# Kernel tuning notes

Measured on AMD Instinct MI355X. Metric: run time of the kernel, lower is better.

## Reference

```python
import jax, jax.numpy as jnp
import numpy as np

B, N, IN, OUT, H, F = 4, 2048, 128, 64, 4, 64


def setup_inputs() -> dict:
    key = jax.random.key(0)
    ks = jax.random.split(key, 10)
    h = jax.random.normal(ks[0], (B, N, IN), dtype=jnp.float32)
    projection_matrix = jax.random.uniform(ks[1], (B, N, N), dtype=jnp.float32)
    similarity_matrix = jnp.tanh(jax.random.normal(ks[2], (B, N, N), dtype=jnp.float32))
    quadrant_matrix = jax.random.randint(ks[3], (B, N, N, 2), 0, 4)
    # learned params (xavier-ish scaling); stored as (in, out) so x @ W
    W = jax.random.normal(ks[4], (IN, OUT * H), dtype=jnp.float32) * (1.0 / np.sqrt(IN))
    random_projection = jax.random.normal(ks[5], (IN, F), dtype=jnp.float32) * 0.1
    a_q = jax.random.normal(ks[6], (2 * F, OUT), dtype=jnp.float32) * (1.0 / np.sqrt(2 * F))
    a_k = jax.random.normal(ks[7], (2 * F, OUT), dtype=jnp.float32) * (1.0 / np.sqrt(2 * F))
    quadrant_bias = jax.random.normal(ks[8], (4, 4), dtype=jnp.float32) * 0.02
    output_proj = jax.random.normal(ks[9], (OUT * H, OUT), dtype=jnp.float32) * (1.0 / np.sqrt(OUT * H))
    return {
        "h": h,
        "projection_matrix": projection_matrix,
        "similarity_matrix": similarity_matrix,
        "W": W,
        "random_projection": random_projection,
        "a_q": a_q,
        "a_k": a_k,
        "quadrant_bias": quadrant_bias,
        "output_proj": output_proj,
        "quadrant_matrix": quadrant_matrix,
    }


def reference(h, projection_matrix, similarity_matrix, W, random_projection,
              a_q, a_k, quadrant_bias, output_proj, quadrant_matrix):
    # random feature map: phi = [cos(h R), sin(h R)]  -> (B, N, 2F)
    proj = jnp.einsum('bnd,df->bnf', h, random_projection)
    phi = jnp.concatenate([jnp.cos(proj), jnp.sin(proj)], axis=-1)
    Q = phi @ a_q                       # (B, N, OUT)
    K = phi @ a_k                       # (B, N, OUT)
    Wh = (h @ W).reshape(h.shape[0], h.shape[1], H, OUT)  # (B, N, H, OUT)

    scores = jnp.einsum('bio,bjo->bij', Q, K)             # (B, N, N)
    # additive relational biases (shared across heads)
    qb = quadrant_bias[quadrant_matrix[..., 0], quadrant_matrix[..., 1]]  # (B, N, N)
    scores = scores + projection_matrix + similarity_matrix + qb
    attn = jax.nn.softmax(scores[:, None, :, :], axis=-1)  # (B, H, N, N) via broadcast

    # aggregate values per head, then concat heads
    hp = jnp.einsum('bhij,bjhk->bihk', attn, Wh)           # (B, N, H, OUT)
    hp = hp.reshape(h.shape[0], h.shape[1], H * OUT)
    out = hp @ output_proj                                  # (B, N, OUT)
    return jax.nn.elu(out)
```

## Files before the change

kernel.cpp:

```cpp
#include <hip/hip_runtime.h>
#include <math.h>

#define BB   4
#define NN   2048
#define IND  128
#define CDIM 256
#define NIT  16

typedef _Float16 half_t;
typedef _Float16 half4_t __attribute__((ext_vector_type(4)));
typedef _Float16 half8_t __attribute__((ext_vector_type(8)));
typedef float    f32x4   __attribute__((ext_vector_type(4)));

#define SHIFT 16.0f

__global__ __launch_bounds__(256) void precompute_kernel(
    const float* __restrict__ hg,
    const float* __restrict__ W,
    const float* __restrict__ R,
    const float* __restrict__ aq,
    const float* __restrict__ ak,
    half_t* __restrict__ Qw,
    half_t* __restrict__ Kw,
    half_t* __restrict__ WhJ)
{
    const int tid  = threadIdx.x;
    const int row0 = blockIdx.x * 8;

    __shared__ float hs[8][IND];
    __shared__ float phis[8][IND];

    {
        const float4* src = (const float4*)(hg + (size_t)row0 * IND);
        ((float4*)&hs[0][0])[tid] = src[tid];
    }
    __syncthreads();

    {
        const int f  = tid & 63;
        const int rr = tid >> 6;
        float p0 = 0.f, p1 = 0.f;
        #pragma unroll 4
        for (int d0 = 0; d0 < IND; d0 += 4) {
            const float r0 = R[(d0 + 0) * 64 + f];
            const float r1 = R[(d0 + 1) * 64 + f];
            const float r2 = R[(d0 + 2) * 64 + f];
            const float r3 = R[(d0 + 3) * 64 + f];
            const float4 ha = *(const float4*)&hs[rr][d0];
            const float4 hb = *(const float4*)&hs[rr + 4][d0];
            p0 += ha.x * r0 + ha.y * r1 + ha.z * r2 + ha.w * r3;
            p1 += hb.x * r0 + hb.y * r1 + hb.z * r2 + hb.w * r3;
        }
        float s, c;
        __sincosf(p0, &s, &c); phis[rr][f]     = c; phis[rr][f + 64]     = s;
        __sincosf(p1, &s, &c); phis[rr + 4][f] = c; phis[rr + 4][f + 64] = s;
    }

    {
        float acc[8];
        #pragma unroll
        for (int r = 0; r < 8; ++r) acc[r] = 0.f;
        #pragma unroll 2
        for (int d0 = 0; d0 < IND; d0 += 4) {
            const float w0 = W[(d0 + 0) * CDIM + tid];
            const float w1 = W[(d0 + 1) * CDIM + tid];
            const float w2 = W[(d0 + 2) * CDIM + tid];
            const float w3 = W[(d0 + 3) * CDIM + tid];
            #pragma unroll
            for (int r = 0; r < 8; ++r) {
                const float4 h4 = *(const float4*)&hs[r][d0];
                acc[r] += h4.x * w0 + h4.y * w1 + h4.z * w2 + h4.w * w3;
            }
        }
        const int b   = row0 >> 11;
        const int j16 = (row0 & (NN - 1)) >> 4;
        const int jr0 = row0 & 8;
        half8_t v;
        #pragma unroll
        for (int r = 0; r < 8; ++r) v[r] = (half_t)acc[r];
        *(half8_t*)(WhJ + (((size_t)b * 128 + j16) * CDIM + tid) * 16 + jr0) = v;
    }
    __syncthreads();

    {
        const int o  = tid & 63;
        const int qk = (tid >> 6) & 1;
        const int rh = tid >> 7;
        const float* A = qk ? ak : aq;
        half_t*    Dst = qk ? Kw : Qw;
        float acc[4] = {0.f, 0.f, 0.f, 0.f};
        #pragma unroll 2
        for (int t0 = 0; t0 < IND; t0 += 4) {
            const float a0 = A[(t0 + 0) * 64 + o];
            const float a1 = A[(t0 + 1) * 64 + o];
            const float a2 = A[(t0 + 2) * 64 + o];
            const float a3 = A[(t0 + 3) * 64 + o];
            #pragma unroll
            for (int r = 0; r < 4; ++r) {
                const float4 ph = *(const float4*)&phis[rh * 4 + r][t0];
                acc[r] += ph.x * a0 + ph.y * a1 + ph.z * a2 + ph.w * a3;
            }
        }
        #pragma unroll
        for (int r = 0; r < 4; ++r)
            Dst[(size_t)(row0 + rh * 4 + r) * 64 + o] = (half_t)acc[r];
    }
}

#define ITER(IT, KC0, KC1, KN0, KN1, PB)                                        \
  {                                                                             \
       \
    const half_t* wpt = wb + (size_t)(IT) * (8 * CDIM * 16);                    \
    half4_t bwv[16];                                                            \
    _Pragma("unroll")                                                           \
    for (int kk = 0; kk < 8; ++kk) {                                            \
      bwv[2 * kk]     = *(const half4_t*)(wpt + (size_t)kk * (CDIM * 16));      \
      bwv[2 * kk + 1] = *(const half4_t*)(wpt + (size_t)kk * (CDIM * 16) + 256);\
    }                                                                           \
                                     \
    f32x4 s4 = (f32x4){0.f, 0.f, 0.f, 0.f};                                     \
    s4 = __builtin_amdgcn_mfma_f32_16x16x32_f16(KC0, qf0, s4, 0, 0, 0);         \
    s4 = __builtin_amdgcn_mfma_f32_16x16x32_f16(KC1, qf1, s4, 0, 0, 0);         \
    if ((IT) + 1 < NIT) {                                                       \
      const half_t* kp = kbase + (size_t)((IT) + 1) * 128 * 64;                 \
      KN0 = *(const half8_t*)(kp + q * 8);                                      \
      KN1 = *(const half8_t*)(kp + 32 + q * 8);                                 \
    }                                                                           \
    const float4 pmC = pmN; const float4 smC = smN;                             \
    const int4 qA = qmN0;  const int4 qB = qmN1;                                \
    if ((IT) + 1 < NIT) {                                                       \
      const int jn = ((IT) + 1) * 128 + cbase;                                  \
      pmN  = *(const float4*)(pmr + jn);                                        \
      smN  = *(const float4*)(smr + jn);                                        \
      qmN0 = *(const int4*)(qmr + (size_t)jn * 2);                              \
      qmN1 = *(const int4*)(qmr + (size_t)jn * 2 + 4);                          \
    }                                                                           \
    const float sv0 = s4[0] + pmC.x + smC.x + qbs[qA.x * 4 + qA.y];             \
    const float sv1 = s4[1] + pmC.y + smC.y + qbs[qA.z * 4 + qA.w];             \
    const float sv2 = s4[2] + pmC.z + smC.z + qbs[qB.x * 4 + qB.y];             \
    const float sv3 = s4[3] + pmC.w + smC.w + qbs[qB.z * 4 + qB.w];             \
    const half_t h0 = (half_t)__expf(fminf(sv0, 11.f));                         \
    const half_t h1 = (half_t)__expf(fminf(sv1, 11.f));                         \
    const half_t h2 = (half_t)__expf(fminf(sv2, 11.f));                         \
    const half_t h3 = (half_t)__expf(fminf(sv3, 11.f));                         \
    half4_t aP; aP[0] = h0; aP[1] = h1; aP[2] = h2; aP[3] = h3;                 \
    lacc += (float)h0 + (float)h1 + (float)h2 + (float)h3;                      \
    *(half4_t*)&Pl[PB][w][lane * 4] = aP;                                       \
    asm volatile("s_waitcnt lgkmcnt(0)" ::: "memory");                          \
    __builtin_amdgcn_s_barrier();                                               \
    asm volatile("" ::: "memory");                                              \
                 \
    _Pragma("unroll")                                                           \
    for (int kk = 0; kk < 8; ++kk) {                                            \
      const half4_t pa = *(const half4_t*)&Pl[PB][kk][lane * 4];                \
      acc0 = __builtin_amdgcn_mfma_f32_16x16x16f16(pa, bwv[2 * kk],     acc0, 0, 0, 0); \
      acc1 = __builtin_amdgcn_mfma_f32_16x16x16f16(pa, bwv[2 * kk + 1], acc1, 0, 0, 0); \
    }                                                                           \
  }

__global__ __launch_bounds__(512, 4) void attn4_kernel(
    const half_t* __restrict__ Qw, const half_t* __restrict__ Kw,
    const half_t* __restrict__ WhJ,
    const float* __restrict__ pm,
    const float* __restrict__ sm,
    const int*   __restrict__ qm,
    const float* __restrict__ qbias,
    const float* __restrict__ op,
    float* __restrict__ out)
{
    const int tid  = threadIdx.x;
    const int w    = tid >> 6;
    const int lane = tid & 63;
    const int n    = lane & 15;
    const int q    = lane >> 4;

    const int blk = blockIdx.x;
    const int b   = (blk & 7) >> 1;
    const int i0  = (((blk >> 3) << 1) | (blk & 1)) * 16;

    __shared__ __align__(16) half_t Pl[2][8][256];
    __shared__ __align__(16) float  BufT0[CDIM][20];
    __shared__ float Lp[8][16];
    __shared__ float qbs[16];

    if (tid < 16) qbs[tid] = qbias[tid] - SHIFT;
    __syncthreads();

    const half_t* qptr = Qw + ((size_t)(b * NN) + i0 + n) * 64;
    const half8_t qf0 = *(const half8_t*)(qptr + q * 8);
    const half8_t qf1 = *(const half8_t*)(qptr + 32 + q * 8);

    const size_t rowoff = ((size_t)b * NN + i0 + n) * NN;
    const float* pmr = pm + rowoff;
    const float* smr = sm + rowoff;
    const int*   qmr = qm + rowoff * 2;
    const int cbase = w * 16 + q * 4;

    const half_t* kbase = Kw + ((size_t)b * NN + w * 16 + n) * 64;
    const half_t* wb = WhJ + ((size_t)b * 128 * CDIM + (size_t)(w * 32 + n)) * 16 + q * 4;

    float4 pmN  = *(const float4*)(pmr + cbase);
    float4 smN  = *(const float4*)(smr + cbase);
    int4   qmN0 = *(const int4*)(qmr + cbase * 2);
    int4   qmN1 = *(const int4*)(qmr + cbase * 2 + 4);
    half8_t ka0 = *(const half8_t*)(kbase + q * 8);
    half8_t ka1 = *(const half8_t*)(kbase + 32 + q * 8);
    half8_t kb0 = ka0, kb1 = ka1;

    f32x4 acc0 = (f32x4){0.f, 0.f, 0.f, 0.f};
    f32x4 acc1 = (f32x4){0.f, 0.f, 0.f, 0.f};
    float lacc = 0.f;

    for (int it = 0; it < NIT; it += 2) {
        ITER(it,     ka0, ka1, kb0, kb1, 0)
        ITER(it + 1, kb0, kb1, ka0, ka1, 1)
    }

    lacc += __shfl_xor(lacc, 16);
    lacc += __shfl_xor(lacc, 32);
    if (lane < 16) Lp[w][lane] = lacc;

    *(f32x4*)&BufT0[w * 32 + n][q * 4]      = acc0;
    *(f32x4*)&BufT0[w * 32 + 16 + n][q * 4] = acc1;
    __syncthreads();

    {
        const int r0 = 2 * w, r1 = 2 * w + 1;
        float pacc0 = 0.f, pacc1 = 0.f;
        #pragma unroll 8
        for (int c = 0; c < CDIM; ++c) {
            const float wv = op[c * 64 + lane];
            pacc0 += BufT0[c][r0] * wv;
            pacc1 += BufT0[c][r1] * wv;
        }
        float lt0 = 0.f, lt1 = 0.f;
        #pragma unroll
        for (int gg = 0; gg < 8; ++gg) { lt0 += Lp[gg][r0]; lt1 += Lp[gg][r1]; }
        float x0 = pacc0 / lt0;
        float x1 = pacc1 / lt1;
        x0 = x0 > 0.f ? x0 : (__expf(x0) - 1.f);
        x1 = x1 > 0.f ? x1 : (__expf(x1) - 1.f);
        out[((size_t)b * NN + i0 + r0) * 64 + lane] = x0;
        out[((size_t)b * NN + i0 + r1) * 64 + lane] = x1;
    }
}

extern "C" void kernel_launch(void* const* d_in, const int* in_sizes, int n_in,
                              void* d_out, int out_size, void* d_ws, size_t ws_size,
                              hipStream_t stream) {
    (void)in_sizes; (void)n_in; (void)out_size; (void)ws_size;
    const float* h  = (const float*)d_in[0];
    const float* pm = (const float*)d_in[1];
    const float* sm = (const float*)d_in[2];
    const float* W  = (const float*)d_in[3];
    const float* R  = (const float*)d_in[4];
    const float* aq = (const float*)d_in[5];
    const float* ak = (const float*)d_in[6];
    const float* qb = (const float*)d_in[7];
    const float* op = (const float*)d_in[8];
    const int*   qm = (const int*)d_in[9];
    float* out = (float*)d_out;

    half_t* ws  = (half_t*)d_ws;
    half_t* Qw  = ws;
    half_t* Kw  = ws + (size_t)BB * NN * 64;
    half_t* WhJ = ws + (size_t)BB * NN * 64 * 2;

    precompute_kernel<<<BB * NN / 8, 256, 0, stream>>>(h, W, R, aq, ak, Qw, Kw, WhJ);
    attn4_kernel<<<BB * (NN / 16), 512, 0, stream>>>(Qw, Kw, WhJ, pm, sm, qm, qb, op, out);
}
```

Baseline: 349.7 us.

## Precombine relational biases into quantized 16-bit buffer in a fused pre-pass

Adds extra blocks to the precompute kernel that stream projection, similarity and quadrant-bias inputs and write their sum as 16-bit fixed-point values into workspace. The attention kernel then reads 2 bytes per score instead of 16, decoding with one fma. This moves bandwidth-heavy, latency-exposed loads out of the MFMA loop into a fully parallel streaming pass, at the cost of extra total traffic, a workspace requirement, and quantization of the bias. The old path is kept as a fallback when the workspace is too small.

```diff
diff --git a/kernel.cpp b/kernel.cpp
--- a/kernel.cpp
+++ b/kernel.cpp
@@ -13,22 +13,58 @@
 typedef float    f32x4   __attribute__((ext_vector_type(4)));
 
 #define SHIFT 16.0f
-
-__global__ __launch_bounds__(256) void precompute_kernel(
+#define BSCL  6.103515625e-05f
+#define BOFF  (-17.5f)
+
+#define NPRE  (BB * NN / 8)
+#define NFUSE 2048
+
+__global__ __launch_bounds__(256) void pre_fuse_kernel(
     const float* __restrict__ hg,
     const float* __restrict__ W,
     const float* __restrict__ R,
     const float* __restrict__ aq,
     const float* __restrict__ ak,
+    const float* __restrict__ pm,
+    const float* __restrict__ sm,
+    const int*   __restrict__ qm,
+    const float* __restrict__ qbias,
     half_t* __restrict__ Qw,
     half_t* __restrict__ Kw,
-    half_t* __restrict__ WhJ)
+    half_t* __restrict__ WhJ,
+    unsigned short* __restrict__ bf)
 {
-    const int tid  = threadIdx.x;
-    const int row0 = blockIdx.x * 8;
+    const int tid = threadIdx.x;
 
     __shared__ float hs[8][IND];
     __shared__ float phis[8][IND];
+    __shared__ float qbs[16];
+
+    if (blockIdx.x >= NPRE) {
+        if (tid < 16) qbs[tid] = qbias[tid];
+        __syncthreads();
+        const int nquad  = BB * NN * NN / 4;
+        const int stride = NFUSE * 256;
+        for (int idx = (blockIdx.x - NPRE) * 256 + tid; idx < nquad; idx += stride) {
+            const float4 p  = ((const float4*)pm)[idx];
+            const float4 s  = ((const float4*)sm)[idx];
+            const int4   qa = ((const int4*)qm)[(size_t)idx * 2];
+            const int4   qb = ((const int4*)qm)[(size_t)idx * 2 + 1];
+            const float f0 = p.x + s.x + qbs[(qa.x << 2) | qa.y];
+            const float f1 = p.y + s.y + qbs[(qa.z << 2) | qa.w];
+            const float f2 = p.z + s.z + qbs[(qb.x << 2) | qb.y];
+            const float f3 = p.w + s.w + qbs[(qb.z << 2) | qb.w];
+            const unsigned u0 = __float2uint_rn(fminf(fmaxf((f0 + 1.5f) * 16384.f, 0.f), 65535.f));
+            const unsigned u1 = __float2uint_rn(fminf(fmaxf((f1 + 1.5f) * 16384.f, 0.f), 65535.f));
+            const unsigned u2 = __float2uint_rn(fminf(fmaxf((f2 + 1.5f) * 16384.f, 0.f), 65535.f));
+            const unsigned u3 = __float2uint_rn(fminf(fmaxf((f3 + 1.5f) * 16384.f, 0.f), 65535.f));
+            uint2 o; o.x = u0 | (u1 << 16); o.y = u2 | (u3 << 16);
+            ((uint2*)bf)[idx] = o;
+        }
+        return;
+    }
+
+    const int row0 = blockIdx.x * 8;
 
     {
         const float4* src = (const float4*)(hg + (size_t)row0 * IND);
@@ -107,7 +143,7 @@
     }
 }
 
-#define ITER(IT, KC0, KC1, KN0, KN1, PB)                                        \
+#define ITERS(IT, KC0, KC1, KN0, KN1, UB, PB)                                   \
   {                                                                             \
        \
     const half_t* wpt = wb + (size_t)(IT) * (8 * CDIM * 16);                    \
@@ -126,19 +162,13 @@
       KN0 = *(const half8_t*)(kp + q * 8);                                      \
       KN1 = *(const half8_t*)(kp + 32 + q * 8);                                 \
     }                                                                           \
-    const float4 pmC = pmN; const float4 smC = smN;                             \
-    const int4 qA = qmN0;  const int4 qB = qmN1;                                \
-    if ((IT) + 1 < NIT) {                                                       \
-      const int jn = ((IT) + 1) * 128 + cbase;                                  \
-      pmN  = *(const float4*)(pmr + jn);                                        \
-      smN  = *(const float4*)(smr + jn);                                        \
-      qmN0 = *(const int4*)(qmr + (size_t)jn * 2);                              \
-      qmN1 = *(const int4*)(qmr + (size_t)jn * 2 + 4);                          \
-    }                                                                           \
-    const float sv0 = s4[0] + pmC.x + smC.x + qbs[qA.x * 4 + qA.y];             \
-    const float sv1 = s4[1] + pmC.y + smC.y + qbs[qA.z * 4 + qA.w];             \
-    const float sv2 = s4[2] + pmC.z + smC.z + qbs[qB.x * 4 + qB.y];             \
-    const float sv3 = s4[3] + pmC.w + smC.w + qbs[qB.z * 4 + qB.w];             \
+    const uint2 uc = UB;                                                        \
+    if ((IT) + 2 < NIT)                                                         \
+      UB = *(const uint2*)(bfr + (size_t)((IT) + 2) * 128 + cbase);             \
+    const float sv0 = s4[0] + fmaf((float)(uc.x & 0xffffu), BSCL, BOFF);        \
+    const float sv1 = s4[1] + fmaf((float)(uc.x >> 16),     BSCL, BOFF);        \
+    const float sv2 = s4[2] + fmaf((float)(uc.y & 0xffffu), BSCL, BOFF);        \
+    const float sv3 = s4[3] + fmaf((float)(uc.y >> 16),     BSCL, BOFF);        \
     const half_t h0 = (half_t)__expf(fminf(sv0, 11.f));                         \
     const half_t h1 = (half_t)__expf(fminf(sv1, 11.f));                         \
     const half_t h2 = (half_t)__expf(fminf(sv2, 11.f));                         \
@@ -158,13 +188,10 @@
     }                                                                           \
   }
 
-__global__ __launch_bounds__(512, 4) void attn4_kernel(
+__global__ __launch_bounds__(512, 4) void attn4s_kernel(
     const half_t* __restrict__ Qw, const half_t* __restrict__ Kw,
     const half_t* __restrict__ WhJ,
-    const float* __restrict__ pm,
-    const float* __restrict__ sm,
-    const int*   __restrict__ qm,
-    const float* __restrict__ qbias,
+    const unsigned short* __restrict__ bf,
     const float* __restrict__ op,
     float* __restrict__ out)
 {
@@ -181,28 +208,20 @@
     __shared__ __align__(16) half_t Pl[2][8][256];
     __shared__ __align__(16) float  BufT0[CDIM][20];
     __shared__ float Lp[8][16];
-    __shared__ float qbs[16];
-
-    if (tid < 16) qbs[tid] = qbias[tid] - SHIFT;
-    __syncthreads();
 
     const half_t* qptr = Qw + ((size_t)(b * NN) + i0 + n) * 64;
     const half8_t qf0 = *(const half8_t*)(qptr + q * 8);
     const half8_t qf1 = *(const half8_t*)(qptr + 32 + q * 8);
 
     const size_t rowoff = ((size_t)b * NN + i0 + n) * NN;
-    const float* pmr = pm + rowoff;
-    const float* smr = sm + rowoff;
-    const int*   qmr = qm + rowoff * 2;
+    const unsigned short* bfr = bf + rowoff;
     const int cbase = w * 16 + q * 4;
 
     const half_t* kbase = Kw + ((size_t)b * NN + w * 16 + n) * 64;
     const half_t* wb = WhJ + ((size_t)b * 128 * CDIM + (size_t)(w * 32 + n)) * 16 + q * 4;
 
-    float4 pmN  = *(const float4*)(pmr + cbase);
-    float4 smN  = *(const float4*)(smr + cbase);
-    int4   qmN0 = *(const int4*)(qmr + cbase * 2);
-    int4   qmN1 = *(const int4*)(qmr + cbase * 2 + 4);
+    uint2 ub0 = *(const uint2*)(bfr + cbase);
+    uint2 ub1 = *(const uint2*)(bfr + 128 + cbase);
     half8_t ka0 = *(const half8_t*)(kbase + q * 8);
     half8_t ka1 = *(const half8_t*)(kbase + 32 + q * 8);
     half8_t kb0 = ka0, kb1 = ka1;
@@ -212,8 +231,8 @@
     float lacc = 0.f;
 
     for (int it = 0; it < NIT; it += 2) {
-        ITER(it,     ka0, ka1, kb0, kb1, 0)
-        ITER(it + 1, kb0, kb1, ka0, ka1, 1)
+        ITERS(it,     ka0, ka1, kb0, kb1, ub0, 0)
+        ITERS(it + 1, kb0, kb1, ka0, ka1, ub1, 1)
     }
 
     lacc += __shfl_xor(lacc, 16);
@@ -245,10 +264,142 @@
     }
 }
 
+#define ITERF(IT, KC0, KC1, KN0, KN1, PB)                                       \
+  {                                                                             \
+    const half_t* wpt = wb + (size_t)(IT) * (8 * CDIM * 16);                    \
+    half4_t bwv[16];                                                            \
+    _Pragma("unroll")                                                           \
+    for (int kk = 0; kk < 8; ++kk) {                                            \
+      bwv[2 * kk]     = *(const half4_t*)(wpt + (size_t)kk * (CDIM * 16));      \
+      bwv[2 * kk + 1] = *(const half4_t*)(wpt + (size_t)kk * (CDIM * 16) + 256);\
+    }                                                                           \
+    f32x4 s4 = (f32x4){0.f, 0.f, 0.f, 0.f};                                     \
+    s4 = __builtin_amdgcn_mfma_f32_16x16x32_f16(KC0, qf0, s4, 0, 0, 0);         \
+    s4 = __builtin_amdgcn_mfma_f32_16x16x32_f16(KC1, qf1, s4, 0, 0, 0);         \
+    if ((IT) + 1 < NIT) {                                                       \
+      const half_t* kp = kbase + (size_t)((IT) + 1) * 128 * 64;                 \
+      KN0 = *(const half8_t*)(kp + q * 8);                                      \
+      KN1 = *(const half8_t*)(kp + 32 + q * 8);                                 \
+    }                                                                           \
+    const float4 pmC = pmN; const float4 smC = smN;                             \
+    const int4 qA = qmN0;  const int4 qB = qmN1;                                \
+    if ((IT) + 1 < NIT) {                                                       \
+      const int jn = ((IT) + 1) * 128 + cbase;                                  \
+      pmN  = *(const float4*)(pmr + jn);                                        \
+      smN  = *(const float4*)(smr + jn);                                        \
+      qmN0 = *(const int4*)(qmr + (size_t)jn * 2);                              \
+      qmN1 = *(const int4*)(qmr + (size_t)jn * 2 + 4);                          \
+    }                                                                           \
+    const float sv0 = s4[0] + pmC.x + smC.x + qbs[qA.x * 4 + qA.y];             \
+    const float sv1 = s4[1] + pmC.y + smC.y + qbs[qA.z * 4 + qA.w];             \
+    const float sv2 = s4[2] + pmC.z + smC.z + qbs[qB.x * 4 + qB.y];             \
+    const float sv3 = s4[3] + pmC.w + smC.w + qbs[qB.z * 4 + qB.w];             \
+    const half_t h0 = (half_t)__expf(fminf(sv0, 11.f));                         \
+    const half_t h1 = (half_t)__expf(fminf(sv1, 11.f));                         \
+    const half_t h2 = (half_t)__expf(fminf(sv2, 11.f));                         \
+    const half_t h3 = (half_t)__expf(fminf(sv3, 11.f));                         \
+    half4_t aP; aP[0] = h0; aP[1] = h1; aP[2] = h2; aP[3] = h3;                 \
+    lacc += (float)h0 + (float)h1 + (float)h2 + (float)h3;                      \
+    *(half4_t*)&Pl[PB][w][lane * 4] = aP;                                       \
+    asm volatile("s_waitcnt lgkmcnt(0)" ::: "memory");                          \
+    __builtin_amdgcn_s_barrier();                                               \
+    asm volatile("" ::: "memory");                                              \
+    _Pragma("unroll")                                                           \
+    for (int kk = 0; kk < 8; ++kk) {                                            \
+      const half4_t pa = *(const half4_t*)&Pl[PB][kk][lane * 4];                \
+      acc0 = __builtin_amdgcn_mfma_f32_16x16x16f16(pa, bwv[2 * kk],     acc0, 0, 0, 0); \
+      acc1 = __builtin_amdgcn_mfma_f32_16x16x16f16(pa, bwv[2 * kk + 1], acc1, 0, 0, 0); \
+    }                                                                           \
+  }
+
+__global__ __launch_bounds__(512, 4) void attn4_kernel(
+    const half_t* __restrict__ Qw, const half_t* __restrict__ Kw,
+    const half_t* __restrict__ WhJ,
+    const float* __restrict__ pm, const float* __restrict__ sm,
+    const int*   __restrict__ qm, const float* __restrict__ qbias,
+    const float* __restrict__ op, float* __restrict__ out)
+{
+    const int tid  = threadIdx.x;
+    const int w    = tid >> 6;
+    const int lane = tid & 63;
+    const int n    = lane & 15;
+    const int q    = lane >> 4;
+
+    const int blk = blockIdx.x;
+    const int b   = (blk & 7) >> 1;
+    const int i0  = (((blk >> 3) << 1) | (blk & 1)) * 16;
+
+    __shared__ __align__(16) half_t Pl[2][8][256];
+    __shared__ __align__(16) float  BufT0[CDIM][20];
+    __shared__ float Lp[8][16];
+    __shared__ float qbs[16];
+
+    if (tid < 16) qbs[tid] = qbias[tid] - SHIFT;
+    __syncthreads();
+
+    const half_t* qptr = Qw + ((size_t)(b * NN) + i0 + n) * 64;
+    const half8_t qf0 = *(const half8_t*)(qptr + q * 8);
+    const half8_t qf1 = *(const half8_t*)(qptr + 32 + q * 8);
+
+    const size_t rowoff = ((size_t)b * NN + i0 + n) * NN;
+    const float* pmr = pm + rowoff;
+    const float* smr = sm + rowoff;
+    const int*   qmr = qm + rowoff * 2;
+    const int cbase = w * 16 + q * 4;
+
+    const half_t* kbase = Kw + ((size_t)b * NN + w * 16 + n) * 64;
+    const half_t* wb = WhJ + ((size_t)b * 128 * CDIM + (size_t)(w * 32 + n)) * 16 + q * 4;
+
+    float4 pmN  = *(const float4*)(pmr + cbase);
+    float4 smN  = *(const float4*)(smr + cbase);
+    int4   qmN0 = *(const int4*)(qmr + cbase * 2);
+    int4   qmN1 = *(const int4*)(qmr + cbase * 2 + 4);
+    half8_t ka0 = *(const half8_t*)(kbase + q * 8);
+    half8_t ka1 = *(const half8_t*)(kbase + 32 + q * 8);
+    half8_t kb0 = ka0, kb1 = ka1;
+
+    f32x4 acc0 = (f32x4){0.f, 0.f, 0.f, 0.f};
+    f32x4 acc1 = (f32x4){0.f, 0.f, 0.f, 0.f};
+    float lacc = 0.f;
+
+    for (int it = 0; it < NIT; it += 2) {
+        ITERF(it,     ka0, ka1, kb0, kb1, 0)
+        ITERF(it + 1, kb0, kb1, ka0, ka1, 1)
+    }
+
+    lacc += __shfl_xor(lacc, 16);
+    lacc += __shfl_xor(lacc, 32);
+    if (lane < 16) Lp[w][lane] = lacc;
+
+    *(f32x4*)&BufT0[w * 32 + n][q * 4]      = acc0;
+    *(f32x4*)&BufT0[w * 32 + 16 + n][q * 4] = acc1;
+    __syncthreads();
+
+    {
+        const int r0 = 2 * w, r1 = 2 * w + 1;
+        float pacc0 = 0.f, pacc1 = 0.f;
+        #pragma unroll 8
+        for (int c = 0; c < CDIM; ++c) {
+            const float wv = op[c * 64 + lane];
+            pacc0 += BufT0[c][r0] * wv;
+            pacc1 += BufT0[c][r1] * wv;
+        }
+        float lt0 = 0.f, lt1 = 0.f;
+        #pragma unroll
+        for (int gg = 0; gg < 8; ++gg) { lt0 += Lp[gg][r0]; lt1 += Lp[gg][r1]; }
+        float x0 = pacc0 / lt0;
+        float x1 = pacc1 / lt1;
+        x0 = x0 > 0.f ? x0 : (__expf(x0) - 1.f);
+        x1 = x1 > 0.f ? x1 : (__expf(x1) - 1.f);
+        out[((size_t)b * NN + i0 + r0) * 64 + lane] = x0;
+        out[((size_t)b * NN + i0 + r1) * 64 + lane] = x1;
+    }
+}
+
 extern "C" void kernel_launch(void* const* d_in, const int* in_sizes, int n_in,
                               void* d_out, int out_size, void* d_ws, size_t ws_size,
                               hipStream_t stream) {
-    (void)in_sizes; (void)n_in; (void)out_size; (void)ws_size;
+    (void)in_sizes; (void)n_in; (void)out_size;
     const float* h  = (const float*)d_in[0];
     const float* pm = (const float*)d_in[1];
     const float* sm = (const float*)d_in[2];
@@ -265,7 +416,19 @@
     half_t* Qw  = ws;
     half_t* Kw  = ws + (size_t)BB * NN * 64;
     half_t* WhJ = ws + (size_t)BB * NN * 64 * 2;
-
-    precompute_kernel<<<BB * NN / 8, 256, 0, stream>>>(h, W, R, aq, ak, Qw, Kw, WhJ);
-    attn4_kernel<<<BB * (NN / 16), 512, 0, stream>>>(Qw, Kw, WhJ, pm, sm, qm, qb, op, out);
+    unsigned short* bf =
+        (unsigned short*)(ws + (size_t)BB * NN * 64 * 2 + (size_t)BB * NN * CDIM);
+
+    const size_t need = ((size_t)BB * NN * 64 * 2 + (size_t)BB * NN * CDIM) * sizeof(half_t)
+                      + (size_t)BB * NN * NN * sizeof(unsigned short);
+
+    if (ws_size >= need) {
+        pre_fuse_kernel<<<NPRE + NFUSE, 256, 0, stream>>>(
+            h, W, R, aq, ak, pm, sm, qm, qb, Qw, Kw, WhJ, bf);
+        attn4s_kernel<<<BB * (NN / 16), 512, 0, stream>>>(Qw, Kw, WhJ, bf, op, out);
+    } else {
+        pre_fuse_kernel<<<NPRE, 256, 0, stream>>>(
+            h, W, R, aq, ak, pm, sm, qm, qb, Qw, Kw, WhJ, bf);
+        attn4_kernel<<<BB * (NN / 16), 512, 0, stream>>>(Qw, Kw, WhJ, pm, sm, qm, qb, op, out);
+    }
 }
```

After: 391.5 us. +11.9%, slower.

## Stage coalesced relational-bias tiles through LDS in fp16 with two-ahead prefetch

Applied to the files above, without the earlier changes.

The projection, similarity and quadrant-index loads are reassigned so that 32 consecutive threads read one 512-byte contiguous row segment. Before, each wave gathered 16 short 64-byte segments from 16 different rows. Each thread combines its three inputs into one fp16 bias value and writes it to a double-buffered LDS tile, which the MFMA lanes read back in their own layout. Loads are issued two iterations ahead. The aim is better coalescing on the dominant memory stream, at the cost of extra LDS traffic and footprint, and rounding the bias to fp16 before the exponent.

```diff
diff --git a/kernel.cpp b/kernel.cpp
--- a/kernel.cpp
+++ b/kernel.cpp
@@ -107,7 +107,7 @@
     }
 }
 
-#define ITER(IT, KC0, KC1, KN0, KN1, PB)                                        \
+#define ITER5(IT, KC0, KC1, KN0, KN1, PB)                                       \
   {                                                                             \
        \
     const half_t* wpt = wb + (size_t)(IT) * (8 * CDIM * 16);                    \
@@ -117,6 +117,22 @@
       bwv[2 * kk]     = *(const half4_t*)(wpt + (size_t)kk * (CDIM * 16));      \
       bwv[2 * kk + 1] = *(const half4_t*)(wpt + (size_t)kk * (CDIM * 16) + 256);\
     }                                                                           \
+            \
+    if ((IT) + 1 < NIT) {                                                       \
+      half4_t hb;                                                               \
+      hb[0] = (half_t)(pmv.x + smv.x + qbs[(qiv0.x << 2) | qiv0.y]);            \
+      hb[1] = (half_t)(pmv.y + smv.y + qbs[(qiv0.z << 2) | qiv0.w]);            \
+      hb[2] = (half_t)(pmv.z + smv.z + qbs[(qiv1.x << 2) | qiv1.y]);            \
+      hb[3] = (half_t)(pmv.w + smv.w + qbs[(qiv1.z << 2) | qiv1.w]);            \
+      *(half4_t*)&Bl[1 - (PB)][str][stc] = hb;                                  \
+    }                                                                           \
+                                  \
+    if ((IT) + 2 < NIT) {                                                       \
+      pmv  = *(const float4*)(pmt + ((IT) + 2) * 128);                          \
+      smv  = *(const float4*)(smt + ((IT) + 2) * 128);                          \
+      qiv0 = *(const int4*)(qmt + (size_t)((IT) + 2) * 256);                    \
+      qiv1 = *(const int4*)(qmt + (size_t)((IT) + 2) * 256 + 4);                \
+    }                                                                           \
                                      \
     f32x4 s4 = (f32x4){0.f, 0.f, 0.f, 0.f};                                     \
     s4 = __builtin_amdgcn_mfma_f32_16x16x32_f16(KC0, qf0, s4, 0, 0, 0);         \
@@ -126,19 +142,12 @@
       KN0 = *(const half8_t*)(kp + q * 8);                                      \
       KN1 = *(const half8_t*)(kp + 32 + q * 8);                                 \
     }                                                                           \
-    const float4 pmC = pmN; const float4 smC = smN;                             \
-    const int4 qA = qmN0;  const int4 qB = qmN1;                                \
-    if ((IT) + 1 < NIT) {                                                       \
-      const int jn = ((IT) + 1) * 128 + cbase;                                  \
-      pmN  = *(const float4*)(pmr + jn);                                        \
-      smN  = *(const float4*)(smr + jn);                                        \
-      qmN0 = *(const int4*)(qmr + (size_t)jn * 2);                              \
-      qmN1 = *(const int4*)(qmr + (size_t)jn * 2 + 4);                          \
-    }                                                                           \
-    const float sv0 = s4[0] + pmC.x + smC.x + qbs[qA.x * 4 + qA.y];             \
-    const float sv1 = s4[1] + pmC.y + smC.y + qbs[qA.z * 4 + qA.w];             \
-    const float sv2 = s4[2] + pmC.z + smC.z + qbs[qB.x * 4 + qB.y];             \
-    const float sv3 = s4[3] + pmC.w + smC.w + qbs[qB.z * 4 + qB.w];             \
+          \
+    const half4_t bh = *(const half4_t*)&Bl[PB][n][cbase];                      \
+    const float sv0 = s4[0] + (float)bh[0] - SHIFT;                             \
+    const float sv1 = s4[1] + (float)bh[1] - SHIFT;                             \
+    const float sv2 = s4[2] + (float)bh[2] - SHIFT;                             \
+    const float sv3 = s4[3] + (float)bh[3] - SHIFT;                             \
     const half_t h0 = (half_t)__expf(fminf(sv0, 11.f));                         \
     const half_t h1 = (half_t)__expf(fminf(sv1, 11.f));                         \
     const half_t h2 = (half_t)__expf(fminf(sv2, 11.f));                         \
@@ -158,7 +167,7 @@
     }                                                                           \
   }
 
-__global__ __launch_bounds__(512, 4) void attn4_kernel(
+__global__ __launch_bounds__(512, 4) void attn5_kernel(
     const half_t* __restrict__ Qw, const half_t* __restrict__ Kw,
     const half_t* __restrict__ WhJ,
     const float* __restrict__ pm,
@@ -179,41 +188,57 @@
     const int i0  = (((blk >> 3) << 1) | (blk & 1)) * 16;
 
     __shared__ __align__(16) half_t Pl[2][8][256];
+    __shared__ __align__(16) half_t Bl[2][16][132];
     __shared__ __align__(16) float  BufT0[CDIM][20];
     __shared__ float Lp[8][16];
     __shared__ float qbs[16];
 
-    if (tid < 16) qbs[tid] = qbias[tid] - SHIFT;
-    __syncthreads();
+    if (tid < 16) qbs[tid] = qbias[tid];
 
     const half_t* qptr = Qw + ((size_t)(b * NN) + i0 + n) * 64;
     const half8_t qf0 = *(const half8_t*)(qptr + q * 8);
     const half8_t qf1 = *(const half8_t*)(qptr + 32 + q * 8);
 
-    const size_t rowoff = ((size_t)b * NN + i0 + n) * NN;
-    const float* pmr = pm + rowoff;
-    const float* smr = sm + rowoff;
-    const int*   qmr = qm + rowoff * 2;
+    const int str = tid >> 5;
+    const int stc = (tid & 31) * 4;
+    const float* pmt = pm + ((size_t)b * NN + i0 + str) * NN + stc;
+    const float* smt = sm + ((size_t)b * NN + i0 + str) * NN + stc;
+    const int*   qmt = qm + (((size_t)b * NN + i0 + str) * NN + stc) * 2;
+
     const int cbase = w * 16 + q * 4;
 
     const half_t* kbase = Kw + ((size_t)b * NN + w * 16 + n) * 64;
     const half_t* wb = WhJ + ((size_t)b * 128 * CDIM + (size_t)(w * 32 + n)) * 16 + q * 4;
 
-    float4 pmN  = *(const float4*)(pmr + cbase);
-    float4 smN  = *(const float4*)(smr + cbase);
-    int4   qmN0 = *(const int4*)(qmr + cbase * 2);
-    int4   qmN1 = *(const int4*)(qmr + cbase * 2 + 4);
+    float4 pmv  = *(const float4*)(pmt);
+    float4 smv  = *(const float4*)(smt);
+    int4   qiv0 = *(const int4*)(qmt);
+    int4   qiv1 = *(const int4*)(qmt + 4);
     half8_t ka0 = *(const half8_t*)(kbase + q * 8);
     half8_t ka1 = *(const half8_t*)(kbase + 32 + q * 8);
     half8_t kb0 = ka0, kb1 = ka1;
+    __syncthreads();
+    {
+        half4_t hb;
+        hb[0] = (half_t)(pmv.x + smv.x + qbs[(qiv0.x << 2) | qiv0.y]);
+        hb[1] = (half_t)(pmv.y + smv.y + qbs[(qiv0.z << 2) | qiv0.w]);
+        hb[2] = (half_t)(pmv.z + smv.z + qbs[(qiv1.x << 2) | qiv1.y]);
+        hb[3] = (half_t)(pmv.w + smv.w + qbs[(qiv1.z << 2) | qiv1.w]);
+        *(half4_t*)&Bl[0][str][stc] = hb;
+    }
+    pmv  = *(const float4*)(pmt + 128);
+    smv  = *(const float4*)(smt + 128);
+    qiv0 = *(const int4*)(qmt + 256);
+    qiv1 = *(const int4*)(qmt + 256 + 4);
+    __syncthreads();
 
     f32x4 acc0 = (f32x4){0.f, 0.f, 0.f, 0.f};
     f32x4 acc1 = (f32x4){0.f, 0.f, 0.f, 0.f};
     float lacc = 0.f;
 
     for (int it = 0; it < NIT; it += 2) {
-        ITER(it,     ka0, ka1, kb0, kb1, 0)
-        ITER(it + 1, kb0, kb1, ka0, ka1, 1)
+        ITER5(it,     ka0, ka1, kb0, kb1, 0)
+        ITER5(it + 1, kb0, kb1, ka0, ka1, 1)
     }
 
     lacc += __shfl_xor(lacc, 16);
@@ -267,5 +292,5 @@
     half_t* WhJ = ws + (size_t)BB * NN * 64 * 2;
 
     precompute_kernel<<<BB * NN / 8, 256, 0, stream>>>(h, W, R, aq, ak, Qw, Kw, WhJ);
-    attn4_kernel<<<BB * (NN / 16), 512, 0, stream>>>(Qw, Kw, WhJ, pm, sm, qm, qb, op, out);
+    attn5_kernel<<<BB * (NN / 16), 512, 0, stream>>>(Qw, Kw, WhJ, pm, sm, qm, qb, op, out);
 }
```

New measurement: 337.7 us. -3.4%, faster.

## Repack Wh tiles for 16-byte B-fragment loads and prefetch bias rows two iterations ahead

Applied to the files above, without the earlier changes.

The precompute kernel now writes Wh in a repacked tile layout, so each lane in the attention kernel loads one 8-half vector per k-step where it previously issued two separate 4-half loads. The attention loop also holds two sets of projection, similarity and quadrant registers and prefetches each set two iterations ahead, giving the large streaming loads more time to arrive. This halves the number of B-operand load instructions and hides more global latency, at the cost of extra registers under the 512x4 launch bound.

```diff
diff --git a/kernel.cpp b/kernel.cpp
--- a/kernel.cpp
+++ b/kernel.cpp
@@ -13,6 +13,7 @@
 typedef float    f32x4   __attribute__((ext_vector_type(4)));
 
 #define SHIFT 16.0f
+
 
 __global__ __launch_bounds__(256) void precompute_kernel(
     const float* __restrict__ hg,
@@ -74,11 +75,20 @@
         }
         const int b   = row0 >> 11;
         const int j16 = (row0 & (NN - 1)) >> 4;
-        const int jr0 = row0 & 8;
-        half8_t v;
-        #pragma unroll
-        for (int r = 0; r < 8; ++r) v[r] = (half_t)acc[r];
-        *(half8_t*)(WhJ + (((size_t)b * 128 + j16) * CDIM + tid) * 16 + jr0) = v;
+        const int jr0 = row0 & 15;
+        const int fp  = tid >> 5;
+        const int hi  = (tid >> 4) & 1;
+        const int nn2 = tid & 15;
+        half_t* tb = WhJ + ((size_t)(b * 128 + j16)) * 4096
+                   + fp * 512 + nn2 * 32 + hi * 4;
+        #pragma unroll
+        for (int rh = 0; rh < 2; ++rh) {
+            const int qv = (jr0 >> 2) + rh;
+            half4_t v;
+            #pragma unroll
+            for (int k = 0; k < 4; ++k) v[k] = (half_t)acc[rh * 4 + k];
+            *(half4_t*)(tb + qv * 8) = v;
+        }
     }
     __syncthreads();
 
@@ -107,16 +117,13 @@
     }
 }
 
-#define ITER(IT, KC0, KC1, KN0, KN1, PB)                                        \
+#define ITER8(IT, KC0, KC1, KN0, KN1, PMV, SMV, QV0, QV1, PB)                   \
   {                                                                             \
-       \
-    const half_t* wpt = wb + (size_t)(IT) * (8 * CDIM * 16);                    \
-    half4_t bwv[16];                                                            \
+          \
+    half8_t bwv[8];                                                             \
     _Pragma("unroll")                                                           \
-    for (int kk = 0; kk < 8; ++kk) {                                            \
-      bwv[2 * kk]     = *(const half4_t*)(wpt + (size_t)kk * (CDIM * 16));      \
-      bwv[2 * kk + 1] = *(const half4_t*)(wpt + (size_t)kk * (CDIM * 16) + 256);\
-    }                                                                           \
+    for (int kq = 0; kq < 8; ++kq)                                              \
+      bwv[kq] = *(const half8_t*)(wb + (size_t)((IT) * 8 + kq) * 4096);         \
                                      \
     f32x4 s4 = (f32x4){0.f, 0.f, 0.f, 0.f};                                     \
     s4 = __builtin_amdgcn_mfma_f32_16x16x32_f16(KC0, qf0, s4, 0, 0, 0);         \
@@ -126,14 +133,15 @@
       KN0 = *(const half8_t*)(kp + q * 8);                                      \
       KN1 = *(const half8_t*)(kp + 32 + q * 8);                                 \
     }                                                                           \
-    const float4 pmC = pmN; const float4 smC = smN;                             \
-    const int4 qA = qmN0;  const int4 qB = qmN1;                                \
-    if ((IT) + 1 < NIT) {                                                       \
-      const int jn = ((IT) + 1) * 128 + cbase;                                  \
-      pmN  = *(const float4*)(pmr + jn);                                        \
-      smN  = *(const float4*)(smr + jn);                                        \
-      qmN0 = *(const int4*)(qmr + (size_t)jn * 2);                              \
-      qmN1 = *(const int4*)(qmr + (size_t)jn * 2 + 4);                          \
+            \
+    const float4 pmC = PMV; const float4 smC = SMV;                             \
+    const int4 qA = QV0;   const int4 qB = QV1;                                 \
+    if ((IT) + 2 < NIT) {                                                       \
+      const int jn = ((IT) + 2) * 128 + cbase;                                  \
+      PMV = *(const float4*)(pmr + jn);                                         \
+      SMV = *(const float4*)(smr + jn);                                         \
+      QV0 = *(const int4*)(qmr + (size_t)jn * 2);                               \
+      QV1 = *(const int4*)(qmr + (size_t)jn * 2 + 4);                           \
     }                                                                           \
     const float sv0 = s4[0] + pmC.x + smC.x + qbs[qA.x * 4 + qA.y];             \
     const float sv1 = s4[1] + pmC.y + smC.y + qbs[qA.z * 4 + qA.w];             \
@@ -151,14 +159,19 @@
     asm volatile("" ::: "memory");                                              \
                  \
     _Pragma("unroll")                                                           \
-    for (int kk = 0; kk < 8; ++kk) {                                            \
-      const half4_t pa = *(const half4_t*)&Pl[PB][kk][lane * 4];                \
-      acc0 = __builtin_amdgcn_mfma_f32_16x16x16f16(pa, bwv[2 * kk],     acc0, 0, 0, 0); \
-      acc1 = __builtin_amdgcn_mfma_f32_16x16x16f16(pa, bwv[2 * kk + 1], acc1, 0, 0, 0); \
+    for (int kq = 0; kq < 8; ++kq) {                                            \
+      const half4_t pa = *(const half4_t*)&Pl[PB][kq][lane * 4];                \
+      half4_t blo, bhi;                                                         \
+      blo[0] = bwv[kq][0]; blo[1] = bwv[kq][1];                                 \
+      blo[2] = bwv[kq][2]; blo[3] = bwv[kq][3];                                 \
+      bhi[0] = bwv[kq][4]; bhi[1] = bwv[kq][5];                                 \
+      bhi[2] = bwv[kq][6]; bhi[3] = bwv[kq][7];                                 \
+      acc0 = __builtin_amdgcn_mfma_f32_16x16x16f16(pa, blo, acc0, 0, 0, 0);     \
+      acc1 = __builtin_amdgcn_mfma_f32_16x16x16f16(pa, bhi, acc1, 0, 0, 0);     \
     }                                                                           \
   }
 
-__global__ __launch_bounds__(512, 4) void attn4_kernel(
+__global__ __launch_bounds__(512, 4) void attn8_kernel(
     const half_t* __restrict__ Qw, const half_t* __restrict__ Kw,
     const half_t* __restrict__ WhJ,
     const float* __restrict__ pm,
@@ -197,12 +210,16 @@
     const int cbase = w * 16 + q * 4;
 
     const half_t* kbase = Kw + ((size_t)b * NN + w * 16 + n) * 64;
-    const half_t* wb = WhJ + ((size_t)b * 128 * CDIM + (size_t)(w * 32 + n)) * 16 + q * 4;
-
-    float4 pmN  = *(const float4*)(pmr + cbase);
-    float4 smN  = *(const float4*)(smr + cbase);
-    int4   qmN0 = *(const int4*)(qmr + cbase * 2);
-    int4   qmN1 = *(const int4*)(qmr + cbase * 2 + 4);
+    const half_t* wb = WhJ + (size_t)b * 128 * 4096 + w * 512 + n * 32 + q * 8;
+
+    float4 pm0  = *(const float4*)(pmr + cbase);
+    float4 sm0  = *(const float4*)(smr + cbase);
+    int4   qa0  = *(const int4*)(qmr + (size_t)cbase * 2);
+    int4   qb0  = *(const int4*)(qmr + (size_t)cbase * 2 + 4);
+    float4 pm1  = *(const float4*)(pmr + 128 + cbase);
+    float4 sm1  = *(const float4*)(smr + 128 + cbase);
+    int4   qa1  = *(const int4*)(qmr + (size_t)(128 + cbase) * 2);
+    int4   qb1  = *(const int4*)(qmr + (size_t)(128 + cbase) * 2 + 4);
     half8_t ka0 = *(const half8_t*)(kbase + q * 8);
     half8_t ka1 = *(const half8_t*)(kbase + 32 + q * 8);
     half8_t kb0 = ka0, kb1 = ka1;
@@ -212,8 +229,8 @@
     float lacc = 0.f;
 
     for (int it = 0; it < NIT; it += 2) {
-        ITER(it,     ka0, ka1, kb0, kb1, 0)
-        ITER(it + 1, kb0, kb1, ka0, ka1, 1)
+        ITER8(it,     ka0, ka1, kb0, kb1, pm0, sm0, qa0, qb0, 0)
+        ITER8(it + 1, kb0, kb1, ka0, ka1, pm1, sm1, qa1, qb1, 1)
     }
 
     lacc += __shfl_xor(lacc, 16);
@@ -267,5 +284,5 @@
     half_t* WhJ = ws + (size_t)BB * NN * 64 * 2;
 
     precompute_kernel<<<BB * NN / 8, 256, 0, stream>>>(h, W, R, aq, ak, Qw, Kw, WhJ);
-    attn4_kernel<<<BB * (NN / 16), 512, 0, stream>>>(Qw, Kw, WhJ, pm, sm, qm, qb, op, out);
+    attn8_kernel<<<BB * (NN / 16), 512, 0, stream>>>(Qw, Kw, WhJ, pm, sm, qm, qb, op, out);
 }
```

New measurement: 395.5 us. 1.13x slower.
